# Optimization experiments

Measured on AMD Instinct MI355X. Metric: run time of the kernel, lower is better.

The kernel has to match this reference:

```python
import jax, jax.numpy as jnp
import numpy as np

B, D_IN, H, D_OUT, E = 16384, 512, 1024, 512, 4


def setup_inputs() -> dict:
    key = jax.random.key(0)
    ks = jax.random.split(key, 8)
    x = jax.random.normal(ks[0], (B, D_IN), dtype=jnp.float32)
    command = jax.random.randint(ks[1], (B,), 0, E, dtype=jnp.int64)
    # Per-branch Encoder params: Linear(D_IN->H), Linear(H->H), Linear(H->D_OUT)
    s = 0.02
    W1 = jax.random.normal(ks[2], (E, D_IN, H), dtype=jnp.float32) * s
    b1 = jnp.zeros((E, H), dtype=jnp.float32)
    W2 = jax.random.normal(ks[3], (E, H, H), dtype=jnp.float32) * s
    b2 = jnp.zeros((E, H), dtype=jnp.float32)
    W3 = jax.random.normal(ks[4], (E, H, D_OUT), dtype=jnp.float32) * s
    b3 = jnp.zeros((E, D_OUT), dtype=jnp.float32)
    return {"x": x, "command": command, "W1": W1, "b1": b1,
            "W2": W2, "b2": b2, "W3": W3, "b3": b3}


def reference(x, command, W1, b1, W2, b2, W3, b3):
    # Evaluate all branches as batched GEMMs, then select per-sample branch.
    # Mathematically identical to per-sample dispatch in the torch module.
    h = jax.nn.relu(jnp.einsum('bi,eih->beh', x, W1) + b1)        # [B,E,H]
    h = jax.nn.relu(jnp.einsum('beh,ehk->bek', h, W2) + b2)       # [B,E,H]
    y = jnp.tanh(jnp.einsum('bek,eko->beo', h, W3) + b3)          # [B,E,D_OUT]
    # select branch output per sample according to command
    idx = command.astype(jnp.int32)[:, None, None]                # [B,1,1]
    out = jnp.take_along_axis(y, idx, axis=1)[:, 0, :]            # [B,D_OUT]
    return out
```

## Files before the change

kernel.cpp:

```cpp
#include <hip/hip_runtime.h>


#define B_N   16384
#define DIN   512
#define HID   1024
#define DOUT  512
#define MAXT256 68
#define MAXT128 136

typedef __attribute__((ext_vector_type(8))) short bf16x8;
typedef __attribute__((ext_vector_type(4))) float f32x4;
typedef __attribute__((address_space(3))) unsigned int lds_u32;
typedef const __attribute__((address_space(1))) unsigned int glb_u32;

__device__ __forceinline__ void gll16(const void* g, void* l) {
    __builtin_amdgcn_global_load_lds((glb_u32*)g, (lds_u32*)l, 16, 0, 0);
}

__device__ __forceinline__ unsigned short f2bf(float f) {
    unsigned int u = __float_as_uint(f);
    u += 0x7FFFu + ((u >> 16) & 1u);
    return (unsigned short)(u >> 16);
}

__device__ __forceinline__ float fast_tanh(float x) {
    x = fminf(fmaxf(x, -9.0f), 9.0f);
    float t = __builtin_amdgcn_exp2f(x * 2.8853900817779268f);
    return (t - 1.0f) * __builtin_amdgcn_rcpf(t + 1.0f);
}

__global__ void plan_all_k(const int* __restrict__ cmd, int* __restrict__ ctrl,
                           int* __restrict__ t256E, int* __restrict__ t256B,
                           int* __restrict__ t128E, int* __restrict__ t128B) {
    __shared__ int h[4];
    int tid = threadIdx.x;
    if (tid < 4) h[tid] = 0;
    __syncthreads();
    int c0 = 0, c1 = 0, c2 = 0, c3 = 0;
    for (int i = tid; i < B_N; i += 256) {
        int e = cmd[i] & 3;
        c0 += (e == 0); c1 += (e == 1); c2 += (e == 2); c3 += (e == 3);
    }
    atomicAdd(&h[0], c0); atomicAdd(&h[1], c1);
    atomicAdd(&h[2], c2); atomicAdd(&h[3], c3);
    __syncthreads();
    if (tid == 0) {
        int P = 0, n256 = 0, n128 = 0;
        for (int e = 0; e < 4; ++e) {
            ctrl[e] = h[e];
            ctrl[4 + e] = 0;
            ctrl[8 + e] = P;
            int cp = ((h[e] + 127) >> 7) << 7;
            int nfull = cp >> 8;
            for (int t = 0; t < nfull; ++t) {
                t256E[n256] = e; t256B[n256] = P + t * 256; ++n256;
            }
            if (cp & 128) {
                t256E[n256] = e | 4; t256B[n256] = P + nfull * 256; ++n256;
            }
            int nt = cp >> 7;
            for (int t = 0; t < nt; ++t) {
                t128E[n128] = e; t128B[n128] = P + t * 128; ++n128;
            }
            P += cp;
        }
        ctrl[12] = P;
        ctrl[13] = n256;
        ctrl[14] = n128;
    }
}

__global__ void scatter_k(const int* __restrict__ cmd, int* __restrict__ ctrl,
                          int* __restrict__ perm) {
    int i = blockIdx.x * 256 + threadIdx.x;
    int e = cmd[i] & 3;
    int lane = threadIdx.x & 63;
#pragma unroll
    for (int ee = 0; ee < 4; ++ee) {
        unsigned long long mask = __ballot(e == ee);
        if (e == ee) {
            int leader = __ffsll((unsigned long long)mask) - 1;
            int rank = __popcll(mask & ((1ull << lane) - 1ull));
            int wbase = 0;
            if (lane == leader)
                wbase = atomicAdd(&ctrl[4 + ee], __popcll(mask));
            wbase = __builtin_amdgcn_readfirstlane(wbase);
            perm[ctrl[8 + ee] + wbase + rank] = i;
        }
    }
}

__global__ __launch_bounds__(256) void prep_data_k(
    const float* __restrict__ W1, const float* __restrict__ W2,
    const float* __restrict__ W3, unsigned short* __restrict__ Wt1,
    unsigned short* __restrict__ Wt2, unsigned short* __restrict__ Wt3,
    const float* __restrict__ x, unsigned short* __restrict__ xp,
    int* __restrict__ perm, const int* __restrict__ ctrl)
{
    int b = blockIdx.x;
    if (b < 8192) {
        int e = b >> 11, r = b & 2047;
        const float* W; unsigned short* Wt; int KD, ND, kt, nt;
        if (r < 512)       { W = W1; Wt = Wt1; KD = 512;  ND = 1024; kt = r & 15;           nt = r >> 4; }
        else if (r < 1536) { W = W2; Wt = Wt2; KD = 1024; ND = 1024; kt = (r - 512) & 31;   nt = (r - 512) >> 5; }
        else               { W = W3; Wt = Wt3; KD = 1024; ND = 512;  kt = (r - 1536) & 31;  nt = (r - 1536) >> 5; }
        __shared__ float t[32][33];
        size_t base = (size_t)e * KD * ND;
        int k0 = kt * 32, n0 = nt * 32;
        int tx = threadIdx.x & 31, ty = threadIdx.x >> 5;
#pragma unroll
        for (int s = 0; s < 4; ++s)
            t[ty + s * 8][tx] = W[base + (size_t)(k0 + ty + s * 8) * ND + n0 + tx];
        __syncthreads();
#pragma unroll
        for (int s = 0; s < 4; ++s)
            Wt[base + (size_t)(n0 + ty + s * 8) * KD + k0 + tx] = f2bf(t[tx][ty + s * 8]);
    } else {
        int g = b - 8192;
        int p = g * 4 + (int)(threadIdx.x >> 6);
        if (p >= ctrl[12]) return;
        int lane = threadIdx.x & 63;
        int e = (p >= ctrl[9]) + (p >= ctrl[10]) + (p >= ctrl[11]);
        int segBase = ctrl[8 + e];
        int src;
        if (p < segBase + ctrl[e]) {
            src = perm[p];
        } else {
            src = perm[segBase];
            if (lane == 0) perm[p] = src;
        }
        const float* xr = x + (size_t)src * DIN + lane * 8;
        float4 a = *(const float4*)xr;
        float4 c = *(const float4*)(xr + 4);
        uint4 o;
        o.x = (unsigned)f2bf(a.x) | ((unsigned)f2bf(a.y) << 16);
        o.y = (unsigned)f2bf(a.z) | ((unsigned)f2bf(a.w) << 16);
        o.z = (unsigned)f2bf(c.x) | ((unsigned)f2bf(c.y) << 16);
        o.w = (unsigned)f2bf(c.z) | ((unsigned)f2bf(c.w) << 16);
        *(uint4*)(xp + (size_t)p * DIN + lane * 8) = o;
    }
}

#define VMW(n) asm volatile("s_waitcnt vmcnt(" #n ")" ::: "memory")
#define BAR  do { asm volatile("" ::: "memory"); __builtin_amdgcn_s_barrier(); \
                  asm volatile("" ::: "memory"); } while (0)

template<int K, int N>
__global__ __launch_bounds__(512, 2) void gemm8_k(
    const unsigned short* __restrict__ A, const unsigned short* __restrict__ Bt,
    const float* __restrict__ bias, unsigned short* __restrict__ Outp,
    const int* __restrict__ ctrl, const int* __restrict__ t256E,
    const int* __restrict__ t256B)
{
    __shared__ unsigned short LDS[65536];
    if ((int)blockIdx.x >= ctrl[13]) return;
    const int te = t256E[blockIdx.x];
    const int e = te & 3;
    const int TM = (te & 4) ? 128 : 256;
    const int wrapMask = TM - 1;
    const int rowBase = t256B[blockIdx.x];
    const int n0 = blockIdx.y * 256;

    const int tid = threadIdx.x;
    const int lane = tid & 63;
    const int w = tid >> 6;
    const int wm = w >> 2, wn = w & 3;
    const int lr = lane & 15, lh = lane >> 4;

    f32x4 acc[2][2][4][2] = {};

    const int tr = tid >> 3, tc = tid & 7;
    const int cs = (tc ^ (tr & 7)) * 8;
    size_t aoff[2][2], boff[2][2];
#pragma unroll
    for (int h = 0; h < 2; ++h)
#pragma unroll
        for (int j = 0; j < 2; ++j) {
            aoff[h][j] = (size_t)(rowBase + ((h * 128 + j * 64 + tr) & wrapMask)) * K + cs;
            boff[h][j] = ((size_t)e * N + n0 + h * 128 + j * 64 + tr) * K + cs;
        }
    const int ksl0 = (lh ^ (lr & 7)) * 8;
    const int ksl1 = ((4 + lh) ^ (lr & 7)) * 8;

#define STAGE_A(tt, h) do { const int _tb = (tt) & 1, _k = (tt) * 64;          \
        gll16(A + aoff[h][0] + _k, &LDS[_tb * 32768 + (h) * 8192 + tid * 8]);  \
        gll16(A + aoff[h][1] + _k, &LDS[_tb * 32768 + (h) * 8192 + 4096 + tid * 8]); } while (0)
#define STAGE_B(tt, h) do { const int _tb = (tt) & 1, _k = (tt) * 64;          \
        gll16(Bt + boff[h][0] + _k, &LDS[_tb * 32768 + 16384 + (h) * 8192 + tid * 8]); \
        gll16(Bt + boff[h][1] + _k, &LDS[_tb * 32768 + 16384 + (h) * 8192 + 4096 + tid * 8]); } while (0)
#define QPHASE(tb, MH, NH) do {                                                \
        bf16x8 afr[4][2], bfr[2][2];                                           \
        _Pragma("unroll") for (int mi = 0; mi < 4; ++mi) {                     \
            int arow = (MH) * 128 + wm * 64 + mi * 16 + lr;                    \
            afr[mi][0] = *(const bf16x8*)&LDS[(tb) * 32768 + arow * 64 + ksl0];\
            afr[mi][1] = *(const bf16x8*)&LDS[(tb) * 32768 + arow * 64 + ksl1];\
        }                                                                      \
        _Pragma("unroll") for (int ni = 0; ni < 2; ++ni) {                     \
            int brow = (NH) * 128 + wn * 32 + ni * 16 + lr;                    \
            bfr[ni][0] = *(const bf16x8*)&LDS[(tb) * 32768 + 16384 + brow * 64 + ksl0]; \
            bfr[ni][1] = *(const bf16x8*)&LDS[(tb) * 32768 + 16384 + brow * 64 + ksl1]; \
        }                                                                      \
        __builtin_amdgcn_s_setprio(1);                                         \
        _Pragma("unroll") for (int mi = 0; mi < 4; ++mi)                       \
        _Pragma("unroll") for (int ni = 0; ni < 2; ++ni) {                     \
            acc[MH][NH][mi][ni] = __builtin_amdgcn_mfma_f32_16x16x32_bf16(     \
                afr[mi][0], bfr[ni][0], acc[MH][NH][mi][ni], 0, 0, 0);         \
            acc[MH][NH][mi][ni] = __builtin_amdgcn_mfma_f32_16x16x32_bf16(     \
                afr[mi][1], bfr[ni][1], acc[MH][NH][mi][ni], 0, 0, 0);         \
        }                                                                      \
        __builtin_amdgcn_s_setprio(0); } while (0)

    constexpr int NT = K / 64;
    STAGE_A(0, 0); STAGE_B(0, 0); STAGE_A(0, 1); STAGE_B(0, 1);
    for (int t = 0; t < NT - 1; ++t) {
        const int tb = t & 1;
        STAGE_A(t + 1, 0); VMW(6); BAR; QPHASE(tb, 0, 0);
        STAGE_B(t + 1, 0); VMW(6); BAR; QPHASE(tb, 1, 0);
        STAGE_A(t + 1, 1); VMW(6); BAR; QPHASE(tb, 0, 1);
        STAGE_B(t + 1, 1);         BAR; QPHASE(tb, 1, 1);
    }
    {
        const int tb = (NT - 1) & 1;
        VMW(4); BAR; QPHASE(tb, 0, 0);
        VMW(2); BAR; QPHASE(tb, 1, 0);
        VMW(0); BAR; QPHASE(tb, 0, 1);
                BAR; QPHASE(tb, 1, 1);
    }
#undef STAGE_A
#undef STAGE_B
#undef QPHASE

#pragma unroll
    for (int mh = 0; mh < 2; ++mh) {
        if (!(TM == 128 && mh == 1)) {
#pragma unroll
            for (int nh = 0; nh < 2; ++nh)
#pragma unroll
                for (int ni = 0; ni < 2; ++ni) {
                    int col = n0 + nh * 128 + wn * 32 + ni * 16 + lr;
                    float bv = bias[e * N + col];
#pragma unroll
                    for (int mi = 0; mi < 4; ++mi)
#pragma unroll
                        for (int r = 0; r < 4; ++r) {
                            int rowL = mh * 128 + wm * 64 + mi * 16 + lh * 4 + r;
                            float v = acc[mh][nh][mi][ni][r] + bv;
                            v = fmaxf(v, 0.0f);
                            Outp[(size_t)(rowBase + rowL) * N + col] = f2bf(v);
                        }
                }
        }
    }
}

template<int K, int N>
__global__ __launch_bounds__(256) void gemm128_k(
    const unsigned short* __restrict__ A, const unsigned short* __restrict__ Bt,
    const float* __restrict__ bias, float* __restrict__ Outp,
    const int* __restrict__ ctrl, const int* __restrict__ t128E,
    const int* __restrict__ t128B, const int* __restrict__ perm)
{
    if ((int)blockIdx.x >= ctrl[14]) return;
    const int e = t128E[blockIdx.x];
    const int rowBase = t128B[blockIdx.x];
    const int n0 = blockIdx.y * 128;

    __shared__ unsigned short Als[128 * 64];
    __shared__ unsigned short Bls[128 * 64];

    const int tid = threadIdx.x;
    const int lane = tid & 63;
    const int w = tid >> 6;
    const int wm = w >> 1, wn = w & 1;
    const int lr = lane & 15, lh = lane >> 4;

    f32x4 acc[4][4] = {};

    const int tr = tid >> 3;
    const int tc = tid & 7;
    const int cs = (tc ^ (tr & 7)) * 8;
    const unsigned short* As = A + (size_t)(rowBase + tr) * K + cs;
    const unsigned short* Bs = Bt + ((size_t)e * N + n0 + tr) * K + cs;
    const int ldst = tr * 64 + tc * 8;

    for (int kq = 0; kq < K / 64; ++kq) {
        const int k0 = kq * 64;
        __syncthreads();
#pragma unroll
        for (int j = 0; j < 4; ++j) {
            gll16(As + (size_t)(j * 32) * K + k0, &Als[j * 2048 + ldst]);
            gll16(Bs + (size_t)(j * 32) * K + k0, &Bls[j * 2048 + ldst]);
        }
        __syncthreads();
#pragma unroll
        for (int kk = 0; kk < 2; ++kk) {
            const int ksl = ((kk * 4 + lh) ^ (lr & 7)) * 8;
            bf16x8 afr[4], bfr[4];
#pragma unroll
            for (int mi = 0; mi < 4; ++mi)
                afr[mi] = *(const bf16x8*)&Als[(wm * 64 + mi * 16 + lr) * 64 + ksl];
#pragma unroll
            for (int ni = 0; ni < 4; ++ni)
                bfr[ni] = *(const bf16x8*)&Bls[(wn * 64 + ni * 16 + lr) * 64 + ksl];
#pragma unroll
            for (int mi = 0; mi < 4; ++mi)
#pragma unroll
                for (int ni = 0; ni < 4; ++ni)
                    acc[mi][ni] = __builtin_amdgcn_mfma_f32_16x16x32_bf16(
                        afr[mi], bfr[ni], acc[mi][ni], 0, 0, 0);
        }
    }

    float bv[4];
    int colv[4];
#pragma unroll
    for (int ni = 0; ni < 4; ++ni) {
        colv[ni] = n0 + wn * 64 + ni * 16 + lr;
        bv[ni] = bias[e * N + colv[ni]];
    }
#pragma unroll
    for (int mi = 0; mi < 4; ++mi) {
#pragma unroll
        for (int r = 0; r < 4; ++r) {
            int rowL = wm * 64 + mi * 16 + lh * 4 + r;
            int orow = perm[rowBase + rowL];
#pragma unroll
            for (int ni = 0; ni < 4; ++ni) {
                float v = fast_tanh(acc[mi][ni][r] + bv[ni]);
                Outp[(size_t)orow * N + colv[ni]] = v;
            }
        }
    }
}

extern "C" void kernel_launch(void* const* d_in, const int* in_sizes, int n_in,
                              void* d_out, int out_size, void* d_ws, size_t ws_size,
                              hipStream_t stream) {
    const float* x  = (const float*)d_in[0];
    const int*   cmd= (const int*)d_in[1];
    const float* W1 = (const float*)d_in[2];
    const float* b1 = (const float*)d_in[3];
    const float* W2 = (const float*)d_in[4];
    const float* b2 = (const float*)d_in[5];
    const float* W3 = (const float*)d_in[6];
    const float* b3 = (const float*)d_in[7];
    float* out = (float*)d_out;

    char* w = (char*)d_ws;
    int* ctrl  = (int*)w;
    int* t256E = ctrl + 64;
    int* t256B = ctrl + 160;
    int* t128E = ctrl + 256;
    int* t128B = ctrl + 448;
    int* perm  = ctrl + 768;
    unsigned short* Wt1 = (unsigned short*)(w + 131072);
    unsigned short* Wt2 = (unsigned short*)(w + 131072 + 4194304);
    unsigned short* Wt3 = (unsigned short*)(w + 131072 + 12582912);
    unsigned short* h1  = (unsigned short*)(w + 131072 + 16777216);
    unsigned short* h2  = h1 + (size_t)16896 * HID;
    unsigned short* xp  = h2;

    plan_all_k<<<1, 256, 0, stream>>>(cmd, ctrl, t256E, t256B, t128E, t128B);
    scatter_k<<<B_N / 256, 256, 0, stream>>>(cmd, ctrl, perm);
    prep_data_k<<<8192 + 4224, 256, 0, stream>>>(W1, W2, W3, Wt1, Wt2, Wt3,
                                                 x, xp, perm, ctrl);

    gemm8_k<DIN, HID><<<dim3(MAXT256, 4), 512, 0, stream>>>(
        xp, Wt1, b1, h1, ctrl, t256E, t256B);
    gemm8_k<HID, HID><<<dim3(MAXT256, 4), 512, 0, stream>>>(
        h1, Wt2, b2, h2, ctrl, t256E, t256B);
    gemm128_k<HID, DOUT><<<dim3(MAXT128, 4), 256, 0, stream>>>(
        h2, Wt3, b3, out, ctrl, t128E, t128B, perm);
}
```

Baseline: 190.6 us.

## Replace double-buffered 256x256 GEMM with simpler 256x128 tile kernel

Replaces the hand-pipelined, double-buffered 256x256-tile GEMM for the first two layers with a single-buffered 256x128-tile kernel that loads each k-slab and syncs twice per iteration. The grid doubles along N and launch bounds allow more blocks per CU, aiming to improve occupancy and parallelism. In exchange it loses the explicit overlap of global loads with MFMA work and halves per-block B reuse.

```diff
diff --git a/kernel.cpp b/kernel.cpp
--- a/kernel.cpp
+++ b/kernel.cpp
@@ -141,25 +141,24 @@
     }
 }
 
-#define VMW(n) asm volatile("s_waitcnt vmcnt(" #n ")" ::: "memory")
-#define BAR  do { asm volatile("" ::: "memory"); __builtin_amdgcn_s_barrier(); \
-                  asm volatile("" ::: "memory"); } while (0)
-
-template<int K, int N>
-__global__ __launch_bounds__(512, 2) void gemm8_k(
+template<int K>
+__global__ __launch_bounds__(512, 4) void gemm256_k(
     const unsigned short* __restrict__ A, const unsigned short* __restrict__ Bt,
     const float* __restrict__ bias, unsigned short* __restrict__ Outp,
     const int* __restrict__ ctrl, const int* __restrict__ t256E,
     const int* __restrict__ t256B)
 {
-    __shared__ unsigned short LDS[65536];
+    constexpr int N = HID;
+    __shared__ unsigned short Als[256 * 64];
+    __shared__ unsigned short Bls[128 * 64];
+
     if ((int)blockIdx.x >= ctrl[13]) return;
     const int te = t256E[blockIdx.x];
     const int e = te & 3;
     const int TM = (te & 4) ? 128 : 256;
     const int wrapMask = TM - 1;
     const int rowBase = t256B[blockIdx.x];
-    const int n0 = blockIdx.y * 256;
+    const int n0 = blockIdx.y * 128;
 
     const int tid = threadIdx.x;
     const int lane = tid & 63;
@@ -167,88 +166,69 @@
     const int wm = w >> 2, wn = w & 3;
     const int lr = lane & 15, lh = lane >> 4;
 
-    f32x4 acc[2][2][4][2] = {};
-
-    const int tr = tid >> 3, tc = tid & 7;
+    f32x4 acc[8][2] = {};
+
+    const int tr = tid >> 3;
+    const int tc = tid & 7;
     const int cs = (tc ^ (tr & 7)) * 8;
-    size_t aoff[2][2], boff[2][2];
-#pragma unroll
-    for (int h = 0; h < 2; ++h)
-#pragma unroll
-        for (int j = 0; j < 2; ++j) {
-            aoff[h][j] = (size_t)(rowBase + ((h * 128 + j * 64 + tr) & wrapMask)) * K + cs;
-            boff[h][j] = ((size_t)e * N + n0 + h * 128 + j * 64 + tr) * K + cs;
-        }
-    const int ksl0 = (lh ^ (lr & 7)) * 8;
-    const int ksl1 = ((4 + lh) ^ (lr & 7)) * 8;
-
-#define STAGE_A(tt, h) do { const int _tb = (tt) & 1, _k = (tt) * 64;          \
-        gll16(A + aoff[h][0] + _k, &LDS[_tb * 32768 + (h) * 8192 + tid * 8]);  \
-        gll16(A + aoff[h][1] + _k, &LDS[_tb * 32768 + (h) * 8192 + 4096 + tid * 8]); } while (0)
-#define STAGE_B(tt, h) do { const int _tb = (tt) & 1, _k = (tt) * 64;          \
-        gll16(Bt + boff[h][0] + _k, &LDS[_tb * 32768 + 16384 + (h) * 8192 + tid * 8]); \
-        gll16(Bt + boff[h][1] + _k, &LDS[_tb * 32768 + 16384 + (h) * 8192 + 4096 + tid * 8]); } while (0)
-#define QPHASE(tb, MH, NH) do {                                                \
-        bf16x8 afr[4][2], bfr[2][2];                                           \
-        _Pragma("unroll") for (int mi = 0; mi < 4; ++mi) {                     \
-            int arow = (MH) * 128 + wm * 64 + mi * 16 + lr;                    \
-            afr[mi][0] = *(const bf16x8*)&LDS[(tb) * 32768 + arow * 64 + ksl0];\
-            afr[mi][1] = *(const bf16x8*)&LDS[(tb) * 32768 + arow * 64 + ksl1];\
-        }                                                                      \
-        _Pragma("unroll") for (int ni = 0; ni < 2; ++ni) {                     \
-            int brow = (NH) * 128 + wn * 32 + ni * 16 + lr;                    \
-            bfr[ni][0] = *(const bf16x8*)&LDS[(tb) * 32768 + 16384 + brow * 64 + ksl0]; \
-            bfr[ni][1] = *(const bf16x8*)&LDS[(tb) * 32768 + 16384 + brow * 64 + ksl1]; \
-        }                                                                      \
-        __builtin_amdgcn_s_setprio(1);                                         \
-        _Pragma("unroll") for (int mi = 0; mi < 4; ++mi)                       \
-        _Pragma("unroll") for (int ni = 0; ni < 2; ++ni) {                     \
-            acc[MH][NH][mi][ni] = __builtin_amdgcn_mfma_f32_16x16x32_bf16(     \
-                afr[mi][0], bfr[ni][0], acc[MH][NH][mi][ni], 0, 0, 0);         \
-            acc[MH][NH][mi][ni] = __builtin_amdgcn_mfma_f32_16x16x32_bf16(     \
-                afr[mi][1], bfr[ni][1], acc[MH][NH][mi][ni], 0, 0, 0);         \
-        }                                                                      \
-        __builtin_amdgcn_s_setprio(0); } while (0)
-
-    constexpr int NT = K / 64;
-    STAGE_A(0, 0); STAGE_B(0, 0); STAGE_A(0, 1); STAGE_B(0, 1);
-    for (int t = 0; t < NT - 1; ++t) {
-        const int tb = t & 1;
-        STAGE_A(t + 1, 0); VMW(6); BAR; QPHASE(tb, 0, 0);
-        STAGE_B(t + 1, 0); VMW(6); BAR; QPHASE(tb, 1, 0);
-        STAGE_A(t + 1, 1); VMW(6); BAR; QPHASE(tb, 0, 1);
-        STAGE_B(t + 1, 1);         BAR; QPHASE(tb, 1, 1);
-    }
-    {
-        const int tb = (NT - 1) & 1;
-        VMW(4); BAR; QPHASE(tb, 0, 0);
-        VMW(2); BAR; QPHASE(tb, 1, 0);
-        VMW(0); BAR; QPHASE(tb, 0, 1);
-                BAR; QPHASE(tb, 1, 1);
-    }
-#undef STAGE_A
-#undef STAGE_B
-#undef QPHASE
-
-#pragma unroll
-    for (int mh = 0; mh < 2; ++mh) {
-        if (!(TM == 128 && mh == 1)) {
-#pragma unroll
-            for (int nh = 0; nh < 2; ++nh)
-#pragma unroll
-                for (int ni = 0; ni < 2; ++ni) {
-                    int col = n0 + nh * 128 + wn * 32 + ni * 16 + lr;
-                    float bv = bias[e * N + col];
-#pragma unroll
-                    for (int mi = 0; mi < 4; ++mi)
-#pragma unroll
-                        for (int r = 0; r < 4; ++r) {
-                            int rowL = mh * 128 + wm * 64 + mi * 16 + lh * 4 + r;
-                            float v = acc[mh][nh][mi][ni][r] + bv;
-                            v = fmaxf(v, 0.0f);
-                            Outp[(size_t)(rowBase + rowL) * N + col] = f2bf(v);
-                        }
-                }
+    const int ldst = tid * 8;
+    int arow[4];
+#pragma unroll
+    for (int j = 0; j < 4; ++j)
+        arow[j] = rowBase + ((j * 64 + tr) & wrapMask);
+    size_t boff[2];
+#pragma unroll
+    for (int j = 0; j < 2; ++j)
+        boff[j] = ((size_t)e * N + n0 + j * 64 + tr) * K + cs;
+
+    for (int kq = 0; kq < K / 64; ++kq) {
+        const int k0 = kq * 64;
+        __syncthreads();
+#pragma unroll
+        for (int j = 0; j < 4; ++j)
+            gll16(A + (size_t)arow[j] * K + cs + k0, &Als[j * 4096 + ldst]);
+#pragma unroll
+        for (int j = 0; j < 2; ++j)
+            gll16(Bt + boff[j] + k0, &Bls[j * 4096 + ldst]);
+        __syncthreads();
+#pragma unroll
+        for (int kk = 0; kk < 2; ++kk) {
+            const int ksl = ((kk * 4 + lh) ^ (lr & 7)) * 8;
+            bf16x8 afr[8], bfr[2];
+#pragma unroll
+            for (int mi = 0; mi < 8; ++mi)
+                afr[mi] = *(const bf16x8*)&Als[(wm * 128 + mi * 16 + lr) * 64 + ksl];
+#pragma unroll
+            for (int ni = 0; ni < 2; ++ni)
+                bfr[ni] = *(const bf16x8*)&Bls[(wn * 32 + ni * 16 + lr) * 64 + ksl];
+#pragma unroll
+            for (int mi = 0; mi < 8; ++mi)
+#pragma unroll
+                for (int ni = 0; ni < 2; ++ni)
+                    acc[mi][ni] = __builtin_amdgcn_mfma_f32_16x16x32_bf16(
+                        afr[mi], bfr[ni], acc[mi][ni], 0, 0, 0);
+        }
+    }
+
+    if (TM == 128 && wm == 1) return;
+    float bv[2];
+    int colv[2];
+#pragma unroll
+    for (int ni = 0; ni < 2; ++ni) {
+        colv[ni] = n0 + wn * 32 + ni * 16 + lr;
+        bv[ni] = bias[e * N + colv[ni]];
+    }
+#pragma unroll
+    for (int mi = 0; mi < 8; ++mi) {
+#pragma unroll
+        for (int r = 0; r < 4; ++r) {
+            int rowL = wm * 128 + mi * 16 + lh * 4 + r;
+            size_t gRow = rowBase + rowL;
+#pragma unroll
+            for (int ni = 0; ni < 2; ++ni) {
+                float v = fmaxf(acc[mi][ni][r] + bv[ni], 0.0f);
+                Outp[gRow * N + colv[ni]] = f2bf(v);
+            }
         }
     }
 }
@@ -365,9 +345,9 @@
     prep_data_k<<<8192 + 4224, 256, 0, stream>>>(W1, W2, W3, Wt1, Wt2, Wt3,
                                                  x, xp, perm, ctrl);
 
-    gemm8_k<DIN, HID><<<dim3(MAXT256, 4), 512, 0, stream>>>(
+    gemm256_k<DIN><<<dim3(MAXT256, 8), 512, 0, stream>>>(
         xp, Wt1, b1, h1, ctrl, t256E, t256B);
-    gemm8_k<HID, HID><<<dim3(MAXT256, 4), 512, 0, stream>>>(
+    gemm256_k<HID><<<dim3(MAXT256, 8), 512, 0, stream>>>(
         h1, Wt2, b2, h2, ctrl, t256E, t256B);
     gemm128_k<HID, DOUT><<<dim3(MAXT128, 4), 256, 0, stream>>>(
         h2, Wt3, b3, out, ctrl, t128E, t128B, perm);
```

Measured after the change: 180.1 us. 1.06x faster.

## Reschedule GEMM pipeline with register fragment reuse and XCD-aware block swizzle

Applied to the files above, without the earlier changes.

Restructures the 8-wave GEMM main loop so the LDS fragment loads are split from the MFMA phases. The quadrant order (00,01,11,10) lets A or B fragments already in registers be reused across consecutive phases, and barriers are placed around each MFMA phase. It also remaps the linear block index with a swizzle that groups the four N-panels of each M-tile together, likely to improve L2 locality across XCDs, and drops the min-2-blocks launch bound. The cost is extra barriers per k-step, and without the occupancy hint register pressure may rise.

```diff
diff --git a/kernel.cpp b/kernel.cpp
--- a/kernel.cpp
+++ b/kernel.cpp
@@ -145,21 +145,26 @@
 #define BAR  do { asm volatile("" ::: "memory"); __builtin_amdgcn_s_barrier(); \
                   asm volatile("" ::: "memory"); } while (0)
 
-template<int K, int N>
-__global__ __launch_bounds__(512, 2) void gemm8_k(
+template<int K>
+__global__ __launch_bounds__(512) void gemm8_k(
     const unsigned short* __restrict__ A, const unsigned short* __restrict__ Bt,
     const float* __restrict__ bias, unsigned short* __restrict__ Outp,
     const int* __restrict__ ctrl, const int* __restrict__ t256E,
     const int* __restrict__ t256B)
 {
+    constexpr int N = HID;
     __shared__ unsigned short LDS[65536];
-    if ((int)blockIdx.x >= ctrl[13]) return;
-    const int te = t256E[blockIdx.x];
+
+    const int l = (int)blockIdx.x + MAXT256 * (int)blockIdx.y;
+    const int swz = (l & 7) * 34 + (l >> 3);
+    const int tile = swz >> 2, panel = swz & 3;
+    if (tile >= ctrl[13]) return;
+    const int te = t256E[tile];
     const int e = te & 3;
     const int TM = (te & 4) ? 128 : 256;
     const int wrapMask = TM - 1;
-    const int rowBase = t256B[blockIdx.x];
-    const int n0 = blockIdx.y * 256;
+    const int rowBase = t256B[tile];
+    const int n0 = panel * 256;
 
     const int tid = threadIdx.x;
     const int lane = tid & 63;
@@ -168,6 +173,7 @@
     const int lr = lane & 15, lh = lane >> 4;
 
     f32x4 acc[2][2][4][2] = {};
+    bf16x8 afr[4][2], bfr[2][2];
 
     const int tr = tid >> 3, tc = tid & 7;
     const int cs = (tc ^ (tr & 7)) * 8;
@@ -182,25 +188,21 @@
     const int ksl0 = (lh ^ (lr & 7)) * 8;
     const int ksl1 = ((4 + lh) ^ (lr & 7)) * 8;
 
-#define STAGE_A(tt, h) do { const int _tb = (tt) & 1, _k = (tt) * 64;          \
-        gll16(A + aoff[h][0] + _k, &LDS[_tb * 32768 + (h) * 8192 + tid * 8]);  \
-        gll16(A + aoff[h][1] + _k, &LDS[_tb * 32768 + (h) * 8192 + 4096 + tid * 8]); } while (0)
-#define STAGE_B(tt, h) do { const int _tb = (tt) & 1, _k = (tt) * 64;          \
-        gll16(Bt + boff[h][0] + _k, &LDS[_tb * 32768 + 16384 + (h) * 8192 + tid * 8]); \
-        gll16(Bt + boff[h][1] + _k, &LDS[_tb * 32768 + 16384 + (h) * 8192 + 4096 + tid * 8]); } while (0)
-#define QPHASE(tb, MH, NH) do {                                                \
-        bf16x8 afr[4][2], bfr[2][2];                                           \
-        _Pragma("unroll") for (int mi = 0; mi < 4; ++mi) {                     \
-            int arow = (MH) * 128 + wm * 64 + mi * 16 + lr;                    \
-            afr[mi][0] = *(const bf16x8*)&LDS[(tb) * 32768 + arow * 64 + ksl0];\
-            afr[mi][1] = *(const bf16x8*)&LDS[(tb) * 32768 + arow * 64 + ksl1];\
-        }                                                                      \
-        _Pragma("unroll") for (int ni = 0; ni < 2; ++ni) {                     \
-            int brow = (NH) * 128 + wn * 32 + ni * 16 + lr;                    \
-            bfr[ni][0] = *(const bf16x8*)&LDS[(tb) * 32768 + 16384 + brow * 64 + ksl0]; \
-            bfr[ni][1] = *(const bf16x8*)&LDS[(tb) * 32768 + 16384 + brow * 64 + ksl1]; \
-        }                                                                      \
-        __builtin_amdgcn_s_setprio(1);                                         \
+#define SA(tt, h) do { const int _tb = ((tt) & 1) * 32768, _k = (tt) * 64;     \
+        gll16(A + aoff[h][0] + _k, &LDS[_tb + (h) * 8192 + tid * 8]);          \
+        gll16(A + aoff[h][1] + _k, &LDS[_tb + (h) * 8192 + 4096 + tid * 8]); } while (0)
+#define SB(tt, h) do { const int _tb = ((tt) & 1) * 32768, _k = (tt) * 64;     \
+        gll16(Bt + boff[h][0] + _k, &LDS[_tb + 16384 + (h) * 8192 + tid * 8]); \
+        gll16(Bt + boff[h][1] + _k, &LDS[_tb + 16384 + (h) * 8192 + 4096 + tid * 8]); } while (0)
+#define LDA(tb, MH) _Pragma("unroll") for (int mi = 0; mi < 4; ++mi) {         \
+        int ar = (MH) * 128 + wm * 64 + mi * 16 + lr;                          \
+        afr[mi][0] = *(const bf16x8*)&LDS[(tb) * 32768 + ar * 64 + ksl0];      \
+        afr[mi][1] = *(const bf16x8*)&LDS[(tb) * 32768 + ar * 64 + ksl1]; }
+#define LDB(tb, NH) _Pragma("unroll") for (int ni = 0; ni < 2; ++ni) {         \
+        int br = (NH) * 128 + wn * 32 + ni * 16 + lr;                          \
+        bfr[ni][0] = *(const bf16x8*)&LDS[(tb) * 32768 + 16384 + br * 64 + ksl0]; \
+        bfr[ni][1] = *(const bf16x8*)&LDS[(tb) * 32768 + 16384 + br * 64 + ksl1]; }
+#define MM(MH, NH) do { __builtin_amdgcn_s_setprio(1);                         \
         _Pragma("unroll") for (int mi = 0; mi < 4; ++mi)                       \
         _Pragma("unroll") for (int ni = 0; ni < 2; ++ni) {                     \
             acc[MH][NH][mi][ni] = __builtin_amdgcn_mfma_f32_16x16x32_bf16(     \
@@ -211,24 +213,29 @@
         __builtin_amdgcn_s_setprio(0); } while (0)
 
     constexpr int NT = K / 64;
-    STAGE_A(0, 0); STAGE_B(0, 0); STAGE_A(0, 1); STAGE_B(0, 1);
-    for (int t = 0; t < NT - 1; ++t) {
+    SA(0, 0); SB(0, 0); SB(0, 1); SA(0, 1);
+    VMW(4); BAR;
+    for (int t = 0; t < NT; ++t) {
         const int tb = t & 1;
-        STAGE_A(t + 1, 0); VMW(6); BAR; QPHASE(tb, 0, 0);
-        STAGE_B(t + 1, 0); VMW(6); BAR; QPHASE(tb, 1, 0);
-        STAGE_A(t + 1, 1); VMW(6); BAR; QPHASE(tb, 0, 1);
-        STAGE_B(t + 1, 1);         BAR; QPHASE(tb, 1, 1);
-    }
-    {
-        const int tb = (NT - 1) & 1;
-        VMW(4); BAR; QPHASE(tb, 0, 0);
-        VMW(2); BAR; QPHASE(tb, 1, 0);
-        VMW(0); BAR; QPHASE(tb, 0, 1);
-                BAR; QPHASE(tb, 1, 1);
-    }
-#undef STAGE_A
-#undef STAGE_B
-#undef QPHASE
+        const bool nl = (t + 1 < NT);
+        LDA(tb, 0); LDB(tb, 0);
+        if (nl) { SA(t + 1, 0); VMW(4); } else { VMW(2); }
+        BAR; MM(0, 0); BAR;
+        LDB(tb, 1);
+        if (nl) { SB(t + 1, 0); VMW(4); } else { VMW(0); }
+        BAR; MM(0, 1); BAR;
+        LDA(tb, 1);
+        if (nl) SB(t + 1, 1);
+        BAR; MM(1, 1); BAR;
+        LDB(tb, 0);
+        if (nl) { SA(t + 1, 1); VMW(4); }
+        BAR; MM(1, 0); BAR;
+    }
+#undef SA
+#undef SB
+#undef LDA
+#undef LDB
+#undef MM
 
 #pragma unroll
     for (int mh = 0; mh < 2; ++mh) {
@@ -365,9 +372,9 @@
     prep_data_k<<<8192 + 4224, 256, 0, stream>>>(W1, W2, W3, Wt1, Wt2, Wt3,
                                                  x, xp, perm, ctrl);
 
-    gemm8_k<DIN, HID><<<dim3(MAXT256, 4), 512, 0, stream>>>(
+    gemm8_k<DIN><<<dim3(MAXT256, 4), 512, 0, stream>>>(
         xp, Wt1, b1, h1, ctrl, t256E, t256B);
-    gemm8_k<HID, HID><<<dim3(MAXT256, 4), 512, 0, stream>>>(
+    gemm8_k<HID><<<dim3(MAXT256, 4), 512, 0, stream>>>(
         h1, Wt2, b2, h2, ctrl, t256E, t256B);
     gemm128_k<HID, DOUT><<<dim3(MAXT128, 4), 256, 0, stream>>>(
         h2, Wt3, b3, out, ctrl, t128E, t128B, perm);
```

Measured after the change: 185.4 us. -2.7%, faster.
